# Kernel optimization log

Hardware: AMD Instinct MI355X
Metric: run time of the kernel (lower is better)

Reference implementation:

```python
import jax, jax.numpy as jnp
import numpy as np

N_NODES = 100000
N_EDGES = 1000000
D = 64            # in_channels == heads*hidden_channels
OUT = 64          # out_channels
L = 3             # local_layers
RVQ = 3           # residual VQ levels per layer
CODES = 16
BN_EPS = 1e-5
COMMIT_W = 0.25


def _l2n(v, eps=1e-12):
    return v / (jnp.linalg.norm(v, axis=-1, keepdims=True) + eps)


def setup_inputs() -> dict:
    key = jax.random.key(0)
    ks = jax.random.split(key, 16)
    s = 1.0 / np.sqrt(D)
    inp = {
        "x": jax.random.normal(ks[0], (N_NODES, D), jnp.float32),
        "edge_index": jax.random.randint(ks[1], (2, N_EDGES), 0, N_NODES, jnp.int64),
        # SAGEConv: lin_l (applied to mean-aggregated neighbors, with bias), lin_r (root, no bias)
        "Wa": jax.random.uniform(ks[2], (L, D, D), jnp.float32, -s, s),
        "ba": jax.random.uniform(ks[3], (L, D), jnp.float32, -s, s),
        "Wr": jax.random.uniform(ks[4], (L, D, D), jnp.float32, -s, s),
        # skip Linear per layer
        "Wl": jax.random.uniform(ks[5], (L, D, D), jnp.float32, -s, s),
        "bl": jax.random.uniform(ks[6], (L, D), jnp.float32, -s, s),
        # BatchNorm affine
        "gamma": jnp.ones((L, D), jnp.float32),
        "beta": jnp.zeros((L, D), jnp.float32),
        # residual-VQ codebooks: [layer, rvq_level, codes, dim]
        "codebooks": jax.random.normal(ks[7], (L, RVQ, CODES, D), jnp.float32),
        # heads
        "Wp": jax.random.uniform(ks[8], (D, OUT), jnp.float32, -s, s),
        "bp": jax.random.uniform(ks[9], (OUT,), jnp.float32, -s, s),
        "Wg": jax.random.uniform(ks[10], (D, L * RVQ), jnp.float32, -s, s),
        "bg": jax.random.uniform(ks[11], (L * RVQ,), jnp.float32, -s, s),
    }
    return inp


def _sage_conv(x, src, dst, Wa, ba, Wr):
    # mean aggregation of source features onto destinations
    summed = jax.ops.segment_sum(x[src], dst, num_segments=N_NODES)
    cnt = jax.ops.segment_sum(jnp.ones((src.shape[0],), x.dtype), dst, num_segments=N_NODES)
    mean = summed / jnp.maximum(cnt, 1.0)[:, None]
    out = mean @ Wa + ba + x @ Wr
    return _l2n(out)  # normalize=True


def _residual_vq(x, cbs):
    # cosine-sim residual VQ, 3 levels; returns (quantized_sum, ids [N,RVQ], commit_loss)
    residual = x
    quant = jnp.zeros_like(x)
    loss = jnp.zeros((), x.dtype)
    ids = []
    for r in range(RVQ):
        cb = _l2n(cbs[r])                       # [CODES, D]
        sim = _l2n(residual) @ cb.T             # [N, CODES]
        idx = jnp.argmax(sim, axis=-1)          # [N]
        q = cb[idx]                             # [N, D]
        loss = loss + COMMIT_W * jnp.mean((jax.lax.stop_gradient(q) - residual) ** 2)
        q_st = residual + jax.lax.stop_gradient(q - residual)  # straight-through
        quant = quant + q_st
        residual = residual - jax.lax.stop_gradient(q)
        ids.append(idx)
    return quant, jnp.stack(ids, axis=1), loss


def reference(x, edge_index, Wa, ba, Wr, Wl, bl, gamma, beta, codebooks, Wp, bp, Wg, bg):
    src, dst = edge_index[0], edge_index[1]
    h = x  # in_dropout: identity at inference
    x_local = jnp.zeros((N_NODES, D), x.dtype)
    total_commit = jnp.zeros((), x.dtype)
    id_list = []
    for i in range(L):
        h = _sage_conv(h, src, dst, Wa[i], ba[i], Wr[i]) + (h @ Wl[i] + bl[i])
        # BatchNorm1d (batch statistics)
        mu = jnp.mean(h, axis=0)
        var = jnp.var(h, axis=0)
        h = (h - mu) * jax.lax.rsqrt(var + BN_EPS) * gamma[i] + beta[i]
        h = jax.nn.relu(h)  # dropout: identity at inference
        x_local = x_local + h
        _, ids, closs = _residual_vq(h, codebooks[i])
        total_commit = total_commit + closs
        id_list.append(ids)
    id_concat = jnp.concatenate(id_list, axis=1)  # [N, L*RVQ]
    gnn_id = x_local @ Wg + bg
    pred = x_local @ Wp + bp
    return (pred, total_commit, id_concat, gnn_id)
```

## Files before the change

kernel.cpp:

```cpp
#include <hip/hip_runtime.h>
#include <math.h>

#define NN 100000
#define NE 1000000
#define D 64
#define L 3
#define RVQ 3
#define CODES 16
#define BN_EPS 1e-5f
#define COMMIT_W 0.25f

#define GRID_A 2048

#define OFS_ROWPTR 0
#define OFS_CNT    100016
#define OFS_CURSOR 200032
#define OFS_BSUMS  300048
#define OFS_BOFFS  300176
#define OFS_STATS  300304
#define OFS_CSR    300800
#define OFS_HA     1300800
#define OFS_HB     7700800
#define OFS_XLOC   14100800
#define OFS_PART   20500800

#define OUT_PRED   0
#define OUT_COMMIT (NN * D)
#define OUT_IDS    (NN * D + 1)
#define OUT_GNN    (NN * D + 1 + NN * (L * RVQ))

static __device__ __forceinline__ float waveSum(float v) {
    #pragma unroll
    for (int off = 32; off; off >>= 1) v += __shfl_xor(v, off, 64);
    return v;
}

static __device__ __forceinline__ float qxor1(float v) {
    return __int_as_float(__builtin_amdgcn_mov_dpp(__float_as_int(v), 0xB1, 0xF, 0xF, 1));
}
static __device__ __forceinline__ float qxor2(float v) {
    return __int_as_float(__builtin_amdgcn_mov_dpp(__float_as_int(v), 0x4E, 0xF, 0xF, 1));
}

__global__ void k_count(const int* __restrict__ dst, int* __restrict__ cnt) {
    int e = blockIdx.x * blockDim.x + threadIdx.x;
    if (e < NE) atomicAdd(&cnt[dst[e]], 1);
}

#define SCAN_B 1024
__global__ void k_scan1(const int* __restrict__ cnt, int* __restrict__ rowptr,
                        int* __restrict__ bsums) {
    __shared__ int sm[SCAN_B];
    int t = threadIdx.x;
    int i = blockIdx.x * SCAN_B + t;
    int v = (i < NN) ? cnt[i] : 0;
    sm[t] = v;
    __syncthreads();
    for (int off = 1; off < SCAN_B; off <<= 1) {
        int add = (t >= off) ? sm[t - off] : 0;
        __syncthreads();
        sm[t] += add;
        __syncthreads();
    }
    if (i < NN) rowptr[i + 1] = sm[t];
    if (t == SCAN_B - 1) bsums[blockIdx.x] = sm[t];
}

__global__ void k_scan2(const int* __restrict__ bsums, int* __restrict__ boffs, int nb) {
    __shared__ int sm[SCAN_B];
    int t = threadIdx.x;
    int orig = (t < nb) ? bsums[t] : 0;
    sm[t] = orig;
    __syncthreads();
    for (int off = 1; off < SCAN_B; off <<= 1) {
        int add = (t >= off) ? sm[t - off] : 0;
        __syncthreads();
        sm[t] += add;
        __syncthreads();
    }
    if (t < nb) boffs[t] = sm[t] - orig;
}

__global__ void k_scan3(int* __restrict__ rowptr, const int* __restrict__ boffs) {
    int i = blockIdx.x * SCAN_B + threadIdx.x;
    if (i < NN) rowptr[i + 1] += boffs[blockIdx.x];
    if (i == 0) rowptr[0] = 0;
}

__global__ void k_cursor(const int* __restrict__ rowptr, int* __restrict__ cursor) {
    int i = blockIdx.x * blockDim.x + threadIdx.x;
    if (i < NN) cursor[i] = rowptr[i];
}

__global__ void k_fill(const int* __restrict__ src, const int* __restrict__ dst,
                       int* __restrict__ cursor, int* __restrict__ csr_src) {
    int e = blockIdx.x * blockDim.x + threadIdx.x;
    if (e < NE) {
        int p = atomicAdd(&cursor[dst[e]], 1);
        csr_src[p] = src[e];
    }
}

__global__ void k_sortrows(const int* __restrict__ rowptr, int* __restrict__ csr) {
    int n = blockIdx.x * blockDim.x + threadIdx.x;
    if (n >= NN) return;
    int r0 = rowptr[n], r1 = rowptr[n + 1];
    for (int i = r0 + 1; i < r1; ++i) {
        int v = csr[i];
        int j = i - 1;
        while (j >= r0 && csr[j] > v) { csr[j + 1] = csr[j]; --j; }
        csr[j + 1] = v;
    }
}

__global__ __launch_bounds__(256) void k_gather(
    const float* __restrict__ h, const int* __restrict__ rowptr,
    const int* __restrict__ csr_src, float* __restrict__ mean_out) {
    int t = threadIdx.x;
    int lane = t & 63, wid = t >> 6;
    int n = blockIdx.x * 4 + wid;
    if (n >= NN) return;

    int r0 = rowptr[n], r1 = rowptr[n + 1];
    float s = 0.f;
    for (int base = r0; base < r1; base += 64) {
        int last = r1 - 1;
        int ii = base + lane;
        int idx = csr_src[(ii <= last) ? ii : last];
        int m = r1 - base;
        if (m > 64) m = 64;
        int j = 0;
        for (; j + 8 <= m; j += 8) {
            int i0 = __shfl(idx, j + 0, 64), i1 = __shfl(idx, j + 1, 64);
            int i2 = __shfl(idx, j + 2, 64), i3 = __shfl(idx, j + 3, 64);
            int i4 = __shfl(idx, j + 4, 64), i5 = __shfl(idx, j + 5, 64);
            int i6 = __shfl(idx, j + 6, 64), i7 = __shfl(idx, j + 7, 64);
            float v0 = h[i0 * D + lane], v1 = h[i1 * D + lane];
            float v2 = h[i2 * D + lane], v3 = h[i3 * D + lane];
            float v4 = h[i4 * D + lane], v5 = h[i5 * D + lane];
            float v6 = h[i6 * D + lane], v7 = h[i7 * D + lane];
            s += v0; s += v1; s += v2; s += v3;
            s += v4; s += v5; s += v6; s += v7;
        }
        for (; j + 4 <= m; j += 4) {
            int i0 = __shfl(idx, j + 0, 64), i1 = __shfl(idx, j + 1, 64);
            int i2 = __shfl(idx, j + 2, 64), i3 = __shfl(idx, j + 3, 64);
            float v0 = h[i0 * D + lane], v1 = h[i1 * D + lane];
            float v2 = h[i2 * D + lane], v3 = h[i3 * D + lane];
            s += v0; s += v1; s += v2; s += v3;
        }
        for (; j < m; ++j) {
            int i0 = __shfl(idx, j, 64);
            s += h[i0 * D + lane];
        }
    }
    float deg = (float)(r1 - r0);
    mean_out[n * D + lane] = s / fmaxf(deg, 1.0f);
}

__global__ __launch_bounds__(256) void k_matvec(
    const float* __restrict__ h, float* __restrict__ hp,
    const float* __restrict__ Wa, const float* __restrict__ ba,
    const float* __restrict__ Wr, const float* __restrict__ Wl,
    const float* __restrict__ bl, float* __restrict__ partials) {
    __shared__ float red[2][4][D];
    __shared__ float lbuf[4][2][128];
    int t = threadIdx.x, lane = t & 63, wid = t >> 6;

    float wa[D], wr[D], wl[D];
    #pragma unroll
    for (int k = 0; k < D; ++k) {
        wa[k] = Wa[k * D + lane];
        wr[k] = Wr[k * D + lane];
        wl[k] = Wl[k * D + lane];
    }
    float bav = ba[lane], blv = bl[lane];

    int wg = blockIdx.x * 4 + wid;
    const int wstep = GRID_A * 4;
    float accS = 0.f, accQ = 0.f;

    int seg = lane >> 4;
    int sl  = lane & 15;

    {
        float4 v = {0.f, 0.f, 0.f, 0.f};
        if (seg == 0)      v = *(const float4*)(hp + (size_t)wg * D + 4 * sl);
        else if (seg == 1) v = *(const float4*)(h  + (size_t)wg * D + 4 * sl);
        if (seg < 2) *(float4*)&lbuf[wid][0][seg * 64 + 4 * sl] = v;
    }

    int p = 0;
    for (int n = wg; n < NN; n += wstep) {
        int nn = n + wstep;
        bool havepf = (nn < NN);
        float4 pf = {0.f, 0.f, 0.f, 0.f};
        if (havepf && seg < 2) {
            const float* srcp = (seg == 0) ? hp : h;
            pf = *(const float4*)(srcp + (size_t)nn * D + 4 * sl);
        }

        const float* mb = &lbuf[wid][p][0];
        const float* hb = &lbuf[wid][p][64];
        float a = 0.f, r = 0.f, lv = 0.f;
        #pragma unroll
        for (int j = 0; j < 16; ++j) {
            float4 m4 = *(const float4*)(mb + 4 * j);
            float4 h4 = *(const float4*)(hb + 4 * j);
            a += m4.x * wa[4 * j + 0]; r += h4.x * wr[4 * j + 0]; lv += h4.x * wl[4 * j + 0];
            a += m4.y * wa[4 * j + 1]; r += h4.y * wr[4 * j + 1]; lv += h4.y * wl[4 * j + 1];
            a += m4.z * wa[4 * j + 2]; r += h4.z * wr[4 * j + 2]; lv += h4.z * wl[4 * j + 2];
            a += m4.w * wa[4 * j + 3]; r += h4.w * wr[4 * j + 3]; lv += h4.w * wl[4 * j + 3];
        }
        float sage = a + bav + r;
        float ss = waveSum(sage * sage);
        float inv = 1.0f / (sqrtf(ss) + 1e-12f);
        float hpv = sage * inv + lv + blv;
        hp[(size_t)n * D + lane] = hpv;
        accS += hpv;
        accQ += hpv * hpv;

        if (havepf && seg < 2)
            *(float4*)&lbuf[wid][p ^ 1][seg * 64 + 4 * sl] = pf;
        p ^= 1;
    }

    red[0][wid][lane] = accS;
    red[1][wid][lane] = accQ;
    __syncthreads();
    if (wid == 0) {
        float s0 = (red[0][0][lane] + red[0][1][lane]) + (red[0][2][lane] + red[0][3][lane]);
        float q0 = (red[1][0][lane] + red[1][1][lane]) + (red[1][2][lane] + red[1][3][lane]);
        partials[blockIdx.x * 128 + lane]      = s0;
        partials[blockIdx.x * 128 + 64 + lane] = q0;
    }
}

__global__ __launch_bounds__(256) void k_red_stats(
    const float* __restrict__ part, float* __restrict__ stats) {
    __shared__ float sm[256];
    int c = blockIdx.x;
    int i = threadIdx.x;
    float s = 0.f;
    #pragma unroll
    for (int k = 0; k < 8; ++k)
        s += part[(size_t)(i * 8 + k) * 128 + c];
    sm[i] = s;
    __syncthreads();
    #pragma unroll
    for (int off = 128; off >= 1; off >>= 1) {
        if (i < off) sm[i] += sm[i + off];
        __syncthreads();
    }
    if (i == 0) stats[c] = sm[0];
}

#define CBSTRIDE 68
__global__ __launch_bounds__(256) void k_layer_b(
    float* __restrict__ hp,
    const float* __restrict__ stats,
    const float* __restrict__ gamma, const float* __restrict__ beta,
    const float* __restrict__ cbs,
    float* __restrict__ x_local,
    float* __restrict__ ids_out,
    int layer, float* __restrict__ commit, int first_layer) {
    __shared__ alignas(16) float scb[RVQ * CODES * CBSTRIDE];
    __shared__ alignas(16) float sscale[D];
    __shared__ alignas(16) float sshift[D];
    __shared__ float sred[4];
    int t = threadIdx.x, lane = t & 63, wid = t >> 6;

    for (int row = wid; row < RVQ * CODES; row += 4) {
        float v = cbs[row * D + lane];
        float ss = waveSum(v * v);
        scb[row * CBSTRIDE + lane] = v / (sqrtf(ss) + 1e-12f);
    }
    if (t < D) {
        float mu = stats[t] * (1.0f / NN);
        float var = stats[64 + t] * (1.0f / NN) - mu * mu;
        float scale = rsqrtf(var + BN_EPS) * gamma[t];
        sscale[t] = scale;
        sshift[t] = beta[t] - mu * scale;
    }
    __syncthreads();

    int gid = blockIdx.x * 256 + t;
    int node = gid >> 2;
    int part = t & 3;
    float closs = 0.f;

    if (node < NN) {
        float res[16];
        size_t base = (size_t)node * D + part * 16;
        const float4* hr = (const float4*)(hp + base);
        float4* hw = (float4*)(hp + base);
        float4* xw = (float4*)(x_local + base);
        const float4* scp = (const float4*)(sscale + part * 16);
        const float4* shp = (const float4*)(sshift + part * 16);

        #pragma unroll
        for (int i = 0; i < 4; ++i) {
            float4 v = hr[i];
            float4 sc = scp[i], sh = shp[i];
            float4 hn;
            hn.x = fmaxf(v.x * sc.x + sh.x, 0.f);
            hn.y = fmaxf(v.y * sc.y + sh.y, 0.f);
            hn.z = fmaxf(v.z * sc.z + sh.z, 0.f);
            hn.w = fmaxf(v.w * sc.w + sh.w, 0.f);
            hw[i] = hn;
            if (first_layer) {
                xw[i] = hn;
            } else {
                float4 xl = xw[i];
                xl.x += hn.x; xl.y += hn.y; xl.z += hn.z; xl.w += hn.w;
                xw[i] = xl;
            }
            res[4 * i + 0] = hn.x; res[4 * i + 1] = hn.y;
            res[4 * i + 2] = hn.z; res[4 * i + 3] = hn.w;
        }

        int bis[RVQ];
        #pragma unroll
        for (int r = 0; r < RVQ; ++r) {
            float sims[CODES];
            #pragma unroll
            for (int j = 0; j < CODES; ++j) {
                const float* cr = &scb[(r * CODES + j) * CBSTRIDE + part * 16];
                float4 c0 = *(const float4*)(cr + 0);
                float4 c1 = *(const float4*)(cr + 4);
                float4 c2 = *(const float4*)(cr + 8);
                float4 c3 = *(const float4*)(cr + 12);
                float a = res[0] * c0.x;
                a += res[1] * c0.y;  a += res[2] * c0.z;  a += res[3] * c0.w;
                a += res[4] * c1.x;  a += res[5] * c1.y;  a += res[6] * c1.z;  a += res[7] * c1.w;
                a += res[8] * c2.x;  a += res[9] * c2.y;  a += res[10] * c2.z; a += res[11] * c2.w;
                a += res[12] * c3.x; a += res[13] * c3.y; a += res[14] * c3.z; a += res[15] * c3.w;
                float b = a + qxor1(a);
                sims[j] = b + qxor2(b);
            }
            float bv = sims[0];
            int bi = 0;
            #pragma unroll
            for (int j = 1; j < CODES; ++j)
                if (sims[j] > bv) { bv = sims[j]; bi = j; }

            const float* qr = &scb[(r * CODES + bi) * CBSTRIDE + part * 16];
            #pragma unroll
            for (int i = 0; i < 4; ++i) {
                float4 q = *(const float4*)(qr + 4 * i);
                float d0 = q.x - res[4 * i + 0]; closs += d0 * d0; res[4 * i + 0] = -d0;
                float d1 = q.y - res[4 * i + 1]; closs += d1 * d1; res[4 * i + 1] = -d1;
                float d2 = q.z - res[4 * i + 2]; closs += d2 * d2; res[4 * i + 2] = -d2;
                float d3 = q.w - res[4 * i + 3]; closs += d3 * d3; res[4 * i + 3] = -d3;
            }
            bis[r] = bi;
        }
        if (part == 0) {
            ids_out[(size_t)node * (L * RVQ) + layer * RVQ + 0] = (float)bis[0];
            ids_out[(size_t)node * (L * RVQ) + layer * RVQ + 1] = (float)bis[1];
            ids_out[(size_t)node * (L * RVQ) + layer * RVQ + 2] = (float)bis[2];
        }
    }

    closs = waveSum(closs);
    if (lane == 0) sred[wid] = closs;
    __syncthreads();
    if (t == 0) {
        float tot = (sred[0] + sred[1]) + (sred[2] + sred[3]);
        atomicAdd(commit, tot * (COMMIT_W / (float)(NN * D)));
    }
}

__global__ __launch_bounds__(256, 2) void k_head(
    const float* __restrict__ x_local,
    const float* __restrict__ Wp, const float* __restrict__ bp,
    const float* __restrict__ Wg, const float* __restrict__ bg,
    float* __restrict__ pred, float* __restrict__ gnn) {
    int t = threadIdx.x, lane = t & 63, wid = t >> 6;
    int jsafe = (lane < 9) ? lane : 0;

    float wp[D], wg[D];
    #pragma unroll
    for (int k = 0; k < D; ++k) {
        wp[k] = Wp[k * D + lane];
        wg[k] = Wg[k * 9 + jsafe];
    }
    float bpv = bp[lane], bgv = bg[jsafe];

    int w = blockIdx.x * 4 + wid;
    int wstep = gridDim.x * 4;
    for (int n = w; n < NN; n += wstep) {
        int nu = __builtin_amdgcn_readfirstlane(n);
        const float4* xrow = (const float4*)(x_local + (size_t)nu * D);
        float p = 0.f, g = 0.f;
        #pragma unroll
        for (int j = 0; j < 16; ++j) {
            float4 x4 = xrow[j];
            p += x4.x * wp[4 * j + 0]; g += x4.x * wg[4 * j + 0];
            p += x4.y * wp[4 * j + 1]; g += x4.y * wg[4 * j + 1];
            p += x4.z * wp[4 * j + 2]; g += x4.z * wg[4 * j + 2];
            p += x4.w * wp[4 * j + 3]; g += x4.w * wg[4 * j + 3];
        }
        pred[(size_t)n * D + lane] = p + bpv;
        if (lane < 9) gnn[(size_t)n * 9 + lane] = g + bgv;
    }
}

extern "C" void kernel_launch(void* const* d_in, const int* in_sizes, int n_in,
                              void* d_out, int out_size, void* d_ws, size_t ws_size,
                              hipStream_t stream) {
    const float* x   = (const float*)d_in[0];
    const int* ei    = (const int*)d_in[1];
    const float* Wa  = (const float*)d_in[2];
    const float* ba  = (const float*)d_in[3];
    const float* Wr  = (const float*)d_in[4];
    const float* Wl  = (const float*)d_in[5];
    const float* bl  = (const float*)d_in[6];
    const float* gamma = (const float*)d_in[7];
    const float* beta  = (const float*)d_in[8];
    const float* cbs = (const float*)d_in[9];
    const float* Wp  = (const float*)d_in[10];
    const float* bp  = (const float*)d_in[11];
    const float* Wg  = (const float*)d_in[12];
    const float* bg  = (const float*)d_in[13];

    const int* src = ei;
    const int* dst = ei + NE;

    int*   ws_i  = (int*)d_ws;
    float* ws_f  = (float*)d_ws;
    int* rowptr  = ws_i + OFS_ROWPTR;
    int* cnt     = ws_i + OFS_CNT;
    int* cursor  = ws_i + OFS_CURSOR;
    int* bsums   = ws_i + OFS_BSUMS;
    int* boffs   = ws_i + OFS_BOFFS;
    float* stats = ws_f + OFS_STATS;
    int* csr_src = ws_i + OFS_CSR;
    float* hA    = ws_f + OFS_HA;
    float* hB    = ws_f + OFS_HB;
    float* xloc  = ws_f + OFS_XLOC;
    float* part  = ws_f + OFS_PART;

    float* out    = (float*)d_out;
    float* pred   = out + OUT_PRED;
    float* commit = out + OUT_COMMIT;
    float* ids    = out + OUT_IDS;
    float* gnn    = out + OUT_GNN;

    hipMemsetAsync(cnt, 0, NN * sizeof(int), stream);
    hipMemsetAsync(commit, 0, sizeof(float), stream);

    k_count<<<(NE + 255) / 256, 256, 0, stream>>>(dst, cnt);
    int nscan = (NN + SCAN_B - 1) / SCAN_B;
    k_scan1<<<nscan, SCAN_B, 0, stream>>>(cnt, rowptr, bsums);
    k_scan2<<<1, SCAN_B, 0, stream>>>(bsums, boffs, nscan);
    k_scan3<<<nscan, SCAN_B, 0, stream>>>(rowptr, boffs);
    k_cursor<<<(NN + 1023) / 1024, 1024, 0, stream>>>(rowptr, cursor);
    k_fill<<<(NE + 255) / 256, 256, 0, stream>>>(src, dst, cursor, csr_src);
    k_sortrows<<<(NN + 255) / 256, 256, 0, stream>>>(rowptr, csr_src);

    const float* hin = x;
    float* bufs[2] = {hA, hB};
    const int nblk_b = (NN * 4 + 255) / 256;
    for (int i = 0; i < L; ++i) {
        float* hp = bufs[i & 1];
        k_gather<<<(NN + 3) / 4, 256, 0, stream>>>(hin, rowptr, csr_src, hp);
        k_matvec<<<GRID_A, 256, 0, stream>>>(hin, hp,
                                             Wa + i * D * D, ba + i * D,
                                             Wr + i * D * D, Wl + i * D * D, bl + i * D,
                                             part);
        k_red_stats<<<128, 256, 0, stream>>>(part, stats + i * 128);
        k_layer_b<<<nblk_b, 256, 0, stream>>>(hp, stats + i * 128,
                                              gamma + i * D, beta + i * D,
                                              cbs + i * RVQ * CODES * D,
                                              xloc, ids, i, commit, (i == 0) ? 1 : 0);
        hin = hp;
    }

    k_head<<<2048, 256, 0, stream>>>(xloc, Wp, bp, Wg, bg, pred, gnn);
}
```

Measured before the change: 851.2 us.

## Stage weights in LDS, process 8 rows per wave, split BN stats into separate kernel

Rewrites the matvec kernel so each block stages all three 64x64 weight matrices in shared memory. Each wave then processes 8 nodes at once, broadcasting input elements with readlane so every weight load from LDS is reused across 8 rows. Previously each thread held 192 weights in registers and streamed one row at a time. BatchNorm sum and sum-of-squares accumulation moves into a new k_bnstats kernel, which adds one extra full read of hp per layer and one more launch.

```diff
diff --git a/kernel.cpp b/kernel.cpp
--- a/kernel.cpp
+++ b/kernel.cpp
@@ -41,6 +41,8 @@
 static __device__ __forceinline__ float qxor2(float v) {
     return __int_as_float(__builtin_amdgcn_mov_dpp(__float_as_int(v), 0x4E, 0xF, 0xF, 1));
 }
+
+#define RLF(v, li) __int_as_float(__builtin_amdgcn_readlane(__float_as_int(v), (li)))
 
 __global__ void k_count(const int* __restrict__ dst, int* __restrict__ cnt) {
     int e = blockIdx.x * blockDim.x + threadIdx.x;
@@ -158,73 +160,87 @@
     mean_out[n * D + lane] = s / fmaxf(deg, 1.0f);
 }
 
-__global__ __launch_bounds__(256) void k_matvec(
+__global__ __launch_bounds__(512, 3) void k_matvec(
     const float* __restrict__ h, float* __restrict__ hp,
     const float* __restrict__ Wa, const float* __restrict__ ba,
     const float* __restrict__ Wr, const float* __restrict__ Wl,
-    const float* __restrict__ bl, float* __restrict__ partials) {
+    const float* __restrict__ bl) {
+    __shared__ float lw[3 * D * D];
+    int t = threadIdx.x, lane = t & 63, wid = t >> 6;
+
+    {
+        float4* d4 = (float4*)lw;
+        const float4* s4;
+        s4 = (const float4*)Wa; d4[t] = s4[t]; d4[t + 512] = s4[t + 512];
+        s4 = (const float4*)Wr; d4[1024 + t] = s4[t]; d4[1024 + t + 512] = s4[t + 512];
+        s4 = (const float4*)Wl; d4[2048 + t] = s4[t]; d4[2048 + t + 512] = s4[t + 512];
+    }
+    __syncthreads();
+
+    int wbase = (blockIdx.x * 8 + wid) * 8;
+    if (wbase >= NN) return;
+
+    float bav = ba[lane], blv = bl[lane];
+
+    const float4* gm = (const float4*)(hp + (size_t)wbase * D);
+    const float4* gh = (const float4*)(h  + (size_t)wbase * D);
+    float4 vm0 = gm[lane], vm1 = gm[lane + 64];
+    float4 vh0 = gh[lane], vh1 = gh[lane + 64];
+    float mreg[8] = {vm0.x, vm0.y, vm0.z, vm0.w, vm1.x, vm1.y, vm1.z, vm1.w};
+    float hreg[8] = {vh0.x, vh0.y, vh0.z, vh0.w, vh1.x, vh1.y, vh1.z, vh1.w};
+
+    float am[8], rm[8], lm[8];
+    #pragma unroll
+    for (int i = 0; i < 8; ++i) { am[i] = 0.f; rm[i] = 0.f; lm[i] = 0.f; }
+
+    #pragma unroll
+    for (int c = 0; c < 4; ++c) {
+        float wa16[16], wr16[16], wl16[16];
+        #pragma unroll
+        for (int j = 0; j < 16; ++j) {
+            wa16[j] = lw[(c * 16 + j) * D + lane];
+            wr16[j] = lw[4096 + (c * 16 + j) * D + lane];
+            wl16[j] = lw[8192 + (c * 16 + j) * D + lane];
+        }
+        #pragma unroll
+        for (int i = 0; i < 8; ++i) {
+            #pragma unroll
+            for (int q = 0; q < 16; ++q) {
+                const int kk = c * 16 + q;
+                const int fid = i * 16 + (kk >> 2);
+                const int rsel = (fid < 64) ? (kk & 3) : 4 + (kk & 3);
+                const int lsel = fid & 63;
+                float mv = RLF(mreg[rsel], lsel);
+                float hv = RLF(hreg[rsel], lsel);
+                am[i] += mv * wa16[q];
+                rm[i] += hv * wr16[q];
+                lm[i] += hv * wl16[q];
+            }
+        }
+    }
+
+    #pragma unroll
+    for (int i = 0; i < 8; ++i) {
+        float sage = am[i] + bav + rm[i];
+        float ss = waveSum(sage * sage);
+        float inv = 1.0f / (sqrtf(ss) + 1e-12f);
+        float hpv = sage * inv + lm[i] + blv;
+        hp[(size_t)(wbase + i) * D + lane] = hpv;
+    }
+}
+
+__global__ __launch_bounds__(256) void k_bnstats(
+    const float* __restrict__ hp, float* __restrict__ partials) {
     __shared__ float red[2][4][D];
-    __shared__ float lbuf[4][2][128];
     int t = threadIdx.x, lane = t & 63, wid = t >> 6;
-
-    float wa[D], wr[D], wl[D];
-    #pragma unroll
-    for (int k = 0; k < D; ++k) {
-        wa[k] = Wa[k * D + lane];
-        wr[k] = Wr[k * D + lane];
-        wl[k] = Wl[k * D + lane];
-    }
-    float bav = ba[lane], blv = bl[lane];
-
     int wg = blockIdx.x * 4 + wid;
     const int wstep = GRID_A * 4;
     float accS = 0.f, accQ = 0.f;
-
-    int seg = lane >> 4;
-    int sl  = lane & 15;
-
-    {
-        float4 v = {0.f, 0.f, 0.f, 0.f};
-        if (seg == 0)      v = *(const float4*)(hp + (size_t)wg * D + 4 * sl);
-        else if (seg == 1) v = *(const float4*)(h  + (size_t)wg * D + 4 * sl);
-        if (seg < 2) *(float4*)&lbuf[wid][0][seg * 64 + 4 * sl] = v;
-    }
-
-    int p = 0;
     for (int n = wg; n < NN; n += wstep) {
-        int nn = n + wstep;
-        bool havepf = (nn < NN);
-        float4 pf = {0.f, 0.f, 0.f, 0.f};
-        if (havepf && seg < 2) {
-            const float* srcp = (seg == 0) ? hp : h;
-            pf = *(const float4*)(srcp + (size_t)nn * D + 4 * sl);
-        }
-
-        const float* mb = &lbuf[wid][p][0];
-        const float* hb = &lbuf[wid][p][64];
-        float a = 0.f, r = 0.f, lv = 0.f;
-        #pragma unroll
-        for (int j = 0; j < 16; ++j) {
-            float4 m4 = *(const float4*)(mb + 4 * j);
-            float4 h4 = *(const float4*)(hb + 4 * j);
-            a += m4.x * wa[4 * j + 0]; r += h4.x * wr[4 * j + 0]; lv += h4.x * wl[4 * j + 0];
-            a += m4.y * wa[4 * j + 1]; r += h4.y * wr[4 * j + 1]; lv += h4.y * wl[4 * j + 1];
-            a += m4.z * wa[4 * j + 2]; r += h4.z * wr[4 * j + 2]; lv += h4.z * wl[4 * j + 2];
-            a += m4.w * wa[4 * j + 3]; r += h4.w * wr[4 * j + 3]; lv += h4.w * wl[4 * j + 3];
-        }
-        float sage = a + bav + r;
-        float ss = waveSum(sage * sage);
-        float inv = 1.0f / (sqrtf(ss) + 1e-12f);
-        float hpv = sage * inv + lv + blv;
-        hp[(size_t)n * D + lane] = hpv;
+        float hpv = hp[(size_t)n * D + lane];
         accS += hpv;
         accQ += hpv * hpv;
-
-        if (havepf && seg < 2)
-            *(float4*)&lbuf[wid][p ^ 1][seg * 64 + 4 * sl] = pf;
-        p ^= 1;
-    }
-
+    }
     red[0][wid][lane] = accS;
     red[1][wid][lane] = accQ;
     __syncthreads();
@@ -461,14 +477,15 @@
 
     const float* hin = x;
     float* bufs[2] = {hA, hB};
-    const int nblk_b = (NN * 4 + 255) / 256;
+    const int nblk_mv = (NN + 63) / 64;
+    const int nblk_b  = (NN * 4 + 255) / 256;
     for (int i = 0; i < L; ++i) {
         float* hp = bufs[i & 1];
         k_gather<<<(NN + 3) / 4, 256, 0, stream>>>(hin, rowptr, csr_src, hp);
-        k_matvec<<<GRID_A, 256, 0, stream>>>(hin, hp,
-                                             Wa + i * D * D, ba + i * D,
-                                             Wr + i * D * D, Wl + i * D * D, bl + i * D,
-                                             part);
+        k_matvec<<<nblk_mv, 512, 0, stream>>>(hin, hp,
+                                              Wa + i * D * D, ba + i * D,
+                                              Wr + i * D * D, Wl + i * D * D, bl + i * D);
+        k_bnstats<<<GRID_A, 256, 0, stream>>>(hp, part);
         k_red_stats<<<128, 256, 0, stream>>>(part, stats + i * 128);
         k_layer_b<<<nblk_b, 256, 0, stream>>>(hp, stats + i * 128,
                                               gamma + i * D, beta + i * D,
```

Measured after the change: 843.1 us. Within noise of the previous version (-1.0%).
